# Kernel tuning notes

Measured on AMD Instinct MI355X. Metric: run time of the kernel, lower is better.

Reference implementation:

```python
import jax, jax.numpy as jnp
import numpy as np

T, B, IN, H, OUT = 128, 1024, 47, 646, 5

def setup_inputs() -> dict:
    key = jax.random.key(0)
    ks = jax.random.split(key, 11)
    s_in = 1.0 / np.sqrt(H)
    return {
        "xs": jax.random.normal(ks[0], (T, B, IN), dtype=jnp.float32),
        "W_ih0": jax.random.normal(ks[1], (H, IN), dtype=jnp.float32) * s_in,
        "W_hh0": jax.random.normal(ks[2], (H, H), dtype=jnp.float32) * s_in,
        "b_ih0": jax.random.normal(ks[3], (H,), dtype=jnp.float32) * s_in,
        "b_hh0": jax.random.normal(ks[4], (H,), dtype=jnp.float32) * s_in,
        "W_ih1": jax.random.normal(ks[5], (H, H), dtype=jnp.float32) * s_in,
        "W_hh1": jax.random.normal(ks[6], (H, H), dtype=jnp.float32) * s_in,
        "b_ih1": jax.random.normal(ks[7], (H,), dtype=jnp.float32) * s_in,
        "b_hh1": jax.random.normal(ks[8], (H,), dtype=jnp.float32) * s_in,
        "W_out": jax.random.normal(ks[9], (OUT, H), dtype=jnp.float32) * s_in,
        "b_out": jnp.zeros((OUT,), dtype=jnp.float32),
    }

def reference(xs, W_ih0, W_hh0, b_ih0, b_hh0, W_ih1, W_hh1, b_ih1, b_hh1, W_out, b_out):
    batch = xs.shape[1]
    h0 = jnp.zeros((batch, H), dtype=xs.dtype)
    h1 = jnp.zeros((batch, H), dtype=xs.dtype)

    def step(carry, x_t):
        h0, h1 = carry
        # layer 0: Elman cell, tanh
        h0 = jnp.tanh(x_t @ W_ih0.T + b_ih0 + h0 @ W_hh0.T + b_hh0)
        # layer 1 consumes layer 0's output at this timestep
        h1 = jnp.tanh(h0 @ W_ih1.T + b_ih1 + h1 @ W_hh1.T + b_hh1)
        return (h0, h1), None

    (h0, h1), _ = jax.lax.scan(step, (h0, h1), xs)
    # classifier on last layer's final hidden state
    logits = h1 @ W_out.T + b_out  # [B, 5]
    return logits
```

## Files before the change

### kernel.cpp

```cpp
#include <hip/hip_runtime.h>
#include <hip/hip_bf16.h>

#define T_STEPS 128
#define B_SZ    1024
#define IN_SZ   47
#define H_SZ    646
#define OUT_SZ  5

#define XK    96
#define K0    768
#define K1    1344
#define N0PAD 704
#define N1PAD 672
#define RING  17
#define SLAB  172032
#define FSTR  256
#define SLOT  16

#define NL0B  7
#define NL1B  14
#define NBLK  (8 * (NL0B + NL1B))

typedef __hip_bfloat16 bf16;
typedef unsigned short ush;
using frag8 = __attribute__((ext_vector_type(8))) short;
using f32x4 = __attribute__((ext_vector_type(4))) float;


__global__ void prep_xs(const float* __restrict__ xs, bf16* __restrict__ xs_pad) {
    int idx = blockIdx.x * blockDim.x + threadIdx.x;
    if (idx >= T_STEPS * B_SZ * XK) return;
    int k = idx % XK;
    int rb = idx / XK;
    float v = (k < IN_SZ) ? xs[(size_t)rb * IN_SZ + k] : 0.f;
    xs_pad[idx] = __float2bfloat16(v);
}

__global__ void pack_w0(const float* __restrict__ Wih, const float* __restrict__ Whh,
                        bf16* __restrict__ Wc) {
    int idx = blockIdx.x * blockDim.x + threadIdx.x;
    if (idx >= N0PAD * K0) return;
    int j = idx / K0, k = idx % K0;
    float v = 0.f;
    if (j < H_SZ) {
        if (k < IN_SZ)                      v = Wih[(size_t)j * IN_SZ + k];
        else if (k >= XK && k < XK + H_SZ)  v = Whh[(size_t)j * H_SZ + (k - XK)];
    }
    Wc[idx] = __float2bfloat16(v);
}

__global__ void pack_w1(const float* __restrict__ Wih, const float* __restrict__ Whh,
                        bf16* __restrict__ Wc) {
    int idx = blockIdx.x * blockDim.x + threadIdx.x;
    if (idx >= N1PAD * K1) return;
    int j = idx / K1, k = idx % K1;
    float v = 0.f;
    if (j < H_SZ) {
        if (k < H_SZ)                          v = Wih[(size_t)j * H_SZ + k];
        else if (k >= 672 && k < 672 + H_SZ)   v = Whh[(size_t)j * H_SZ + (k - 672)];
    }
    Wc[idx] = __float2bfloat16(v);
}

__global__ void pack_bias(const float* __restrict__ bi, const float* __restrict__ bh,
                          float* __restrict__ b, int n) {
    int j = blockIdx.x * blockDim.x + threadIdx.x;
    if (j >= n) return;
    b[j] = (j < H_SZ) ? (bi[j] + bh[j]) : 0.f;
}


__device__ __forceinline__ void tanh_store(ush* dst, float x) {
    x = fminf(fmaxf(x, -15.f), 15.f);
    float e = __expf(2.f * x);
    bf16 hb = __float2bfloat16((e - 1.f) / (e + 1.f));
    *dst = *(ush*)&hb;
}

__device__ __forceinline__ void poll_ge(int* p, int need) {
    while (__hip_atomic_load(p, __ATOMIC_RELAXED, __HIP_MEMORY_SCOPE_AGENT) < need)
        __builtin_amdgcn_s_sleep(2);
}

__global__ __launch_bounds__(512, 2) void persist(
    const bf16* __restrict__ xs_pad, const bf16* __restrict__ Wc0,
    const bf16* __restrict__ Wc1, const float* __restrict__ b0,
    const float* __restrict__ b1, bf16* __restrict__ Sring,
    int* __restrict__ flags)
{
    extern __shared__ ush Wlds[];
    const int bid  = blockIdx.x;
    const int rg   = bid & 7;
    const int c8   = bid >> 3;
    const bool isL0 = (c8 < NL0B);
    const int tid  = threadIdx.x;
    const int wv   = tid >> 6;
    const int lane = tid & 63;
    const int q8   = (lane >> 4) * 8;
    const int l15  = lane & 15;

    if (isL0) {
        const int col0 = c8 * 96;
        for (int g = wv; g < 144; g += 8) {
            int kc = g / 6, ct = g % 6;
            const bf16* src = Wc0 + (size_t)(col0 + ct*16 + l15) * K0 + kc*32 + q8;
            *(uint4*)&Wlds[g*512 + lane*8] = *(const uint4*)src;
        }
    } else {
        const int col0 = (c8 - NL0B) * 48;
        for (int g = wv; g < 126; g += 8) {
            int kc = g / 3, ct = g % 3;
            const bf16* src = Wc1 + (size_t)(col0 + ct*16 + l15) * K1 + kc*32 + q8;
            *(uint4*)&Wlds[g*512 + lane*8] = *(const uint4*)src;
        }
    }
    __syncthreads();

    const int loc = wv * 16 + l15;
    bf16* const ringbase = Sring + (size_t)rg * RING * SLAB;
    int*  const fL0 = flags + rg * FSTR;
    int*  const fL1 = flags + (8 + rg) * FSTR;

    if (isL0) {
        const int col0 = c8 * 96;
        float bias[6];
        #pragma unroll
        for (int ct = 0; ct < 6; ++ct) bias[ct] = b0[col0 + ct*16 + l15];

        for (int p = 0; p < 128; ++p) {
            const bf16* rsl = ringbase + (size_t)((p + RING - 1) % RING) * SLAB;
            bf16*       wsl = ringbase + (size_t)(p % RING) * SLAB;

            const bf16* xr = xs_pad + ((size_t)p * B_SZ + rg*128 + loc) * XK + q8;
            uint4 xbuf[3];
            #pragma unroll
            for (int i = 0; i < 3; ++i) xbuf[i] = *(const uint4*)(xr + i*32);

            if (wv == 0) {
                int* addr = nullptr; int need = 0;
                if (p > 0 && lane < NL0B)            { addr = &fL0[lane * SLOT];        need = p; }
                else if (p >= RING && lane >= 16 && lane < 16 + NL1B)
                                                     { addr = &fL1[(lane - 16) * SLOT]; need = p - 16; }
                if (addr) poll_ge(addr, need);
            }
            __syncthreads();
            if (p >= RING + 1 && (p - 1) % RING == 0)
                __builtin_amdgcn_fence(__ATOMIC_ACQUIRE, "agent");

            const bf16* hr = rsl + (size_t)loc * K1 + q8;
            uint4 hbuf[21];
            #pragma unroll
            for (int i = 0; i < 21; ++i) hbuf[i] = *(const uint4*)(hr + i*32);

            f32x4 acc[6] = {};
            #pragma unroll
            for (int kc = 0; kc < 24; ++kc) {
                frag8 af = (kc < 3) ? *(const frag8*)&xbuf[kc]
                                    : *(const frag8*)&hbuf[kc-3];
                #pragma unroll
                for (int ct = 0; ct < 6; ++ct) {
                    frag8 wf = *(const frag8*)&Wlds[(kc*6+ct)*512 + lane*8];
                    acc[ct] = __builtin_amdgcn_mfma_f32_16x16x32_bf16(
                        af, wf, acc[ct], 0, 0, 0);
                }
            }
            const int rbase = wv*16 + (lane>>4)*4;
            #pragma unroll
            for (int ct = 0; ct < 6; ++ct) {
                const int col = col0 + ct*16 + l15;
                if (col < H_SZ) {
                    #pragma unroll
                    for (int i = 0; i < 4; ++i)
                        tanh_store((ush*)(wsl + (size_t)(rbase+i)*K1 + col),
                                   acc[ct][i] + bias[ct]);
                }
            }
            __syncthreads();
            if (tid == 0)
                __hip_atomic_store(&fL0[c8 * SLOT], p + 1, __ATOMIC_RELAXED,
                                   __HIP_MEMORY_SCOPE_AGENT);
        }
    } else {
        const int col0 = (c8 - NL0B) * 48;
        const int myslot = (c8 - NL0B) * SLOT;
        float bias[3];
        #pragma unroll
        for (int ct = 0; ct < 3; ++ct) bias[ct] = b1[col0 + ct*16 + l15];

        for (int q = 1; q <= 128; ++q) {
            const bf16* rsl = ringbase + (size_t)((q + RING - 1) % RING) * SLAB;
            bf16*       wsl = ringbase + (size_t)(q % RING) * SLAB;
            const bf16* ar  = rsl + (size_t)loc * K1 + q8;

            if (wv == 0 && lane < NL0B) poll_ge(&fL0[lane * SLOT], q);
            __syncthreads();
            if (q >= RING + 1 && (q - 1) % RING == 0)
                __builtin_amdgcn_fence(__ATOMIC_ACQUIRE, "agent");

            uint4 h0buf[21];
            #pragma unroll
            for (int i = 0; i < 21; ++i) h0buf[i] = *(const uint4*)(ar + i*32);
            f32x4 acc[3] = {};
            #pragma unroll
            for (int kc = 0; kc < 21; ++kc) {
                frag8 af = *(const frag8*)&h0buf[kc];
                #pragma unroll
                for (int ct = 0; ct < 3; ++ct) {
                    frag8 wf = *(const frag8*)&Wlds[(kc*3+ct)*512 + lane*8];
                    acc[ct] = __builtin_amdgcn_mfma_f32_16x16x32_bf16(
                        af, wf, acc[ct], 0, 0, 0);
                }
            }

            if (q > 1) {
                if (wv == 0 && lane < NL1B) poll_ge(&fL1[lane * SLOT], q - 1);
                __syncthreads();
            }
            uint4 h1buf[21];
            #pragma unroll
            for (int i = 0; i < 21; ++i)
                h1buf[i] = *(const uint4*)(ar + (21 + i)*32);
            #pragma unroll
            for (int kc = 21; kc < 42; ++kc) {
                frag8 af = *(const frag8*)&h1buf[kc-21];
                #pragma unroll
                for (int ct = 0; ct < 3; ++ct) {
                    frag8 wf = *(const frag8*)&Wlds[(kc*3+ct)*512 + lane*8];
                    acc[ct] = __builtin_amdgcn_mfma_f32_16x16x32_bf16(
                        af, wf, acc[ct], 0, 0, 0);
                }
            }
            const int rbase = wv*16 + (lane>>4)*4;
            #pragma unroll
            for (int ct = 0; ct < 3; ++ct) {
                const int col = col0 + ct*16 + l15;
                if (col < H_SZ) {
                    #pragma unroll
                    for (int i = 0; i < 4; ++i)
                        tanh_store((ush*)(wsl + (size_t)(rbase+i)*K1 + 672 + col),
                                   acc[ct][i] + bias[ct]);
                }
            }
            __syncthreads();
            if (tid == 0)
                __hip_atomic_store(&fL1[myslot], q, __ATOMIC_RELAXED,
                                   __HIP_MEMORY_SCOPE_AGENT);
        }
    }
}

__global__ __launch_bounds__(256) void classifier(
    const bf16* __restrict__ Sring, const float* __restrict__ Wout,
    const float* __restrict__ bout, float* __restrict__ out)
{
    const int wave = threadIdx.x >> 6, lane = threadIdx.x & 63;
    const int row = blockIdx.x * 4 + wave;
    const int rg = row >> 7, loc = row & 127;
    const bf16* h1 = Sring + ((size_t)rg * RING + (128 % RING)) * SLAB
                     + (size_t)loc * K1 + 672;
    float acc[OUT_SZ] = {0.f, 0.f, 0.f, 0.f, 0.f};
    for (int k = lane; k < H_SZ; k += 64) {
        float h = __bfloat162float(h1[k]);
        #pragma unroll
        for (int o = 0; o < OUT_SZ; ++o) acc[o] += h * Wout[(size_t)o * H_SZ + k];
    }
    #pragma unroll
    for (int o = 0; o < OUT_SZ; ++o) {
        float v = acc[o];
        #pragma unroll
        for (int off = 32; off; off >>= 1) v += __shfl_down(v, off, 64);
        if (lane == 0) out[(size_t)row * OUT_SZ + o] = v + bout[o];
    }
}


extern "C" void kernel_launch(void* const* d_in, const int* in_sizes, int n_in,
                              void* d_out, int out_size, void* d_ws, size_t ws_size,
                              hipStream_t stream) {
    const float* xs   = (const float*)d_in[0];
    const float* Wih0 = (const float*)d_in[1];
    const float* Whh0 = (const float*)d_in[2];
    const float* bih0 = (const float*)d_in[3];
    const float* bhh0 = (const float*)d_in[4];
    const float* Wih1 = (const float*)d_in[5];
    const float* Whh1 = (const float*)d_in[6];
    const float* bih1 = (const float*)d_in[7];
    const float* bhh1 = (const float*)d_in[8];
    const float* Wout = (const float*)d_in[9];
    const float* bout = (const float*)d_in[10];
    float* out = (float*)d_out;

    char* ws = (char*)d_ws;
    size_t off = 0;
    bf16* xs_pad = (bf16*)(ws + off); off += (size_t)T_STEPS * B_SZ * XK * 2;
    bf16* Wc0    = (bf16*)(ws + off); off += (size_t)N0PAD * K0 * 2;
    bf16* Wc1    = (bf16*)(ws + off); off += (size_t)N1PAD * K1 * 2;
    float* b0    = (float*)(ws + off); off += (size_t)N0PAD * 4;
    float* b1    = (float*)(ws + off); off += (size_t)N1PAD * 4;
    bf16* Sring  = (bf16*)(ws + off); off += (size_t)8 * RING * SLAB * 2;
    int*  flags  = (int*)(ws + off);  off += (size_t)16 * FSTR * 4;

    hipMemsetAsync(Sring, 0, (size_t)8 * RING * SLAB * 2, stream);
    hipMemsetAsync(flags, 0, (size_t)16 * FSTR * 4, stream);

    prep_xs <<<(T_STEPS * B_SZ * XK + 255) / 256, 256, 0, stream>>>(xs, xs_pad);
    pack_w0 <<<(N0PAD * K0 + 255) / 256, 256, 0, stream>>>(Wih0, Whh0, Wc0);
    pack_w1 <<<(N1PAD * K1 + 255) / 256, 256, 0, stream>>>(Wih1, Whh1, Wc1);
    pack_bias<<<(N0PAD + 255) / 256, 256, 0, stream>>>(bih0, bhh0, b0, N0PAD);
    pack_bias<<<(N1PAD + 255) / 256, 256, 0, stream>>>(bih1, bhh1, b1, N1PAD);

    hipFuncSetAttribute((const void*)persist,
                        hipFuncAttributeMaxDynamicSharedMemorySize, 147456);
    void* args[] = { (void*)&xs_pad, (void*)&Wc0, (void*)&Wc1, (void*)&b0,
                     (void*)&b1, (void*)&Sring, (void*)&flags };
    hipLaunchCooperativeKernel((const void*)persist, dim3(NBLK), dim3(512),
                               args, 147456, stream);

    classifier<<<B_SZ / 4, 256, 0, stream>>>(Sring, Wout, bout, out);
}
```

Baseline: 1.607 ms.

## Replace block-wide barriers with per-wave flags for inter-block step synchronization

Each wave now owns a slice of 16 batch rows and publishes and polls its own progress flags, so cross-block dependencies are tracked per wave rather than per block. The __syncthreads calls around polling and flag publication are removed, and each wave waits on its own stores with s_waitcnt before lane 0 sets the flag. This is meant to drop block-wide barrier stalls and let waves run ahead independently. In exchange it adds eight times more flags and more polling traffic, and correctness relies on the relaxed store ordering. The ring-reuse wait for layer 0 also changes from p-16 to p-RING+1.

```diff
diff --git a/kernel.cpp b/kernel.cpp
--- a/kernel.cpp
+++ b/kernel.cpp
@@ -118,8 +118,8 @@
 
     const int loc = wv * 16 + l15;
     bf16* const ringbase = Sring + (size_t)rg * RING * SLAB;
-    int*  const fL0 = flags + rg * FSTR;
-    int*  const fL1 = flags + (8 + rg) * FSTR;
+    int* const fL0w = flags + ((rg * 2 + 0) * 8 + wv) * FSTR;
+    int* const fL1w = flags + ((rg * 2 + 1) * 8 + wv) * FSTR;
 
     if (isL0) {
         const int col0 = c8 * 96;
@@ -136,14 +136,13 @@
             #pragma unroll
             for (int i = 0; i < 3; ++i) xbuf[i] = *(const uint4*)(xr + i*32);
 
-            if (wv == 0) {
+            {
                 int* addr = nullptr; int need = 0;
-                if (p > 0 && lane < NL0B)            { addr = &fL0[lane * SLOT];        need = p; }
+                if (p > 0 && lane < NL0B)      { addr = &fL0w[lane * SLOT];        need = p; }
                 else if (p >= RING && lane >= 16 && lane < 16 + NL1B)
-                                                     { addr = &fL1[(lane - 16) * SLOT]; need = p - 16; }
+                                               { addr = &fL1w[(lane - 16) * SLOT]; need = p - RING + 1; }
                 if (addr) poll_ge(addr, need);
             }
-            __syncthreads();
             if (p >= RING + 1 && (p - 1) % RING == 0)
                 __builtin_amdgcn_fence(__ATOMIC_ACQUIRE, "agent");
 
@@ -175,9 +174,9 @@
                                    acc[ct][i] + bias[ct]);
                 }
             }
-            __syncthreads();
-            if (tid == 0)
-                __hip_atomic_store(&fL0[c8 * SLOT], p + 1, __ATOMIC_RELAXED,
+            asm volatile("s_waitcnt vmcnt(0)" ::: "memory");
+            if (lane == 0)
+                __hip_atomic_store(&fL0w[c8 * SLOT], p + 1, __ATOMIC_RELAXED,
                                    __HIP_MEMORY_SCOPE_AGENT);
         }
     } else {
@@ -192,8 +191,7 @@
             bf16*       wsl = ringbase + (size_t)(q % RING) * SLAB;
             const bf16* ar  = rsl + (size_t)loc * K1 + q8;
 
-            if (wv == 0 && lane < NL0B) poll_ge(&fL0[lane * SLOT], q);
-            __syncthreads();
+            if (lane < NL0B) poll_ge(&fL0w[lane * SLOT], q);
             if (q >= RING + 1 && (q - 1) % RING == 0)
                 __builtin_amdgcn_fence(__ATOMIC_ACQUIRE, "agent");
 
@@ -212,10 +210,7 @@
                 }
             }
 
-            if (q > 1) {
-                if (wv == 0 && lane < NL1B) poll_ge(&fL1[lane * SLOT], q - 1);
-                __syncthreads();
-            }
+            if (q > 1 && lane < NL1B) poll_ge(&fL1w[lane * SLOT], q - 1);
             uint4 h1buf[21];
             #pragma unroll
             for (int i = 0; i < 21; ++i)
@@ -241,9 +236,9 @@
                                    acc[ct][i] + bias[ct]);
                 }
             }
-            __syncthreads();
-            if (tid == 0)
-                __hip_atomic_store(&fL1[myslot], q, __ATOMIC_RELAXED,
+            asm volatile("s_waitcnt vmcnt(0)" ::: "memory");
+            if (lane == 0)
+                __hip_atomic_store(&fL1w[myslot], q, __ATOMIC_RELAXED,
                                    __HIP_MEMORY_SCOPE_AGENT);
         }
     }
@@ -298,10 +293,10 @@
     float* b0    = (float*)(ws + off); off += (size_t)N0PAD * 4;
     float* b1    = (float*)(ws + off); off += (size_t)N1PAD * 4;
     bf16* Sring  = (bf16*)(ws + off); off += (size_t)8 * RING * SLAB * 2;
-    int*  flags  = (int*)(ws + off);  off += (size_t)16 * FSTR * 4;
+    int*  flags  = (int*)(ws + off);  off += (size_t)(8 * 2 * 8) * FSTR * 4;
 
     hipMemsetAsync(Sring, 0, (size_t)8 * RING * SLAB * 2, stream);
-    hipMemsetAsync(flags, 0, (size_t)16 * FSTR * 4, stream);
+    hipMemsetAsync(flags, 0, (size_t)(8 * 2 * 8) * FSTR * 4, stream);
 
     prep_xs <<<(T_STEPS * B_SZ * XK + 255) / 256, 256, 0, stream>>>(xs, xs_pad);
     pack_w0 <<<(N0PAD * K0 + 255) / 256, 256, 0, stream>>>(Wih0, Whh0, Wc0);
```

Measured after the change: 1.611 ms. About the same (+0.2%).
